# Kernel optimization log

Hardware: AMD Instinct MI355X
Metric: run time of the kernel (lower is better)

The kernel has to match this reference:

```python
import jax, jax.numpy as jnp
import numpy as np

HEAD_SIZE = 128
BLOCK_SIZE = 2048


def setup_inputs() -> dict:
    key = jax.random.key(0)
    kx, kk, kq, kv = jax.random.split(key, 4)
    B, T, C = 8, 2048, HEAD_SIZE
    s = 1.0 / np.sqrt(C)
    x = jax.random.normal(kx, (B, T, C), dtype=jnp.float32)
    Wk = jax.random.normal(kk, (C, C), dtype=jnp.float32) * s
    Wq = jax.random.normal(kq, (C, C), dtype=jnp.float32) * s
    Wv = jax.random.normal(kv, (C, C), dtype=jnp.float32) * s
    return {"x": x, "Wk": Wk, "Wq": Wq, "Wv": Wv}


def reference(x, Wk, Wq, Wv):
    B, T, C = x.shape
    # nn.Linear(C, C, bias=False): y = x @ W.T
    k = jnp.einsum('btc,dc->btd', x, Wk)
    q = jnp.einsum('btc,dc->btd', x, Wq)
    v = jnp.einsum('btc,dc->btd', x, Wv)
    scores = jnp.einsum('btd,bsd->bts', q, k) * (C ** -0.5)  # [B,T,T]
    causal = jnp.tril(jnp.ones((T, T), dtype=bool))
    scores = jnp.where(causal, scores, -jnp.inf)
    weights = jax.nn.softmax(scores, axis=-1)
    return jnp.einsum('bts,bsd->btd', weights, v)
```

## Files before the change

kernel.cpp:

```cpp
#include <hip/hip_runtime.h>

#define T_SEQ 2048
#define C_DIM 128
#define S_QK 0.08838834764831845f

typedef __attribute__((ext_vector_type(8))) short bf16x8;
typedef __attribute__((ext_vector_type(4))) float f32x4;

#define OPART_OFF 12582912UL
#define ML_OFF    31457280UL

#define GLOAD_LDS16(gp, lp)                                          \
    __builtin_amdgcn_global_load_lds(                                \
        (const __attribute__((address_space(1))) void*)(gp),         \
        (__attribute__((address_space(3))) void*)(lp), 16, 0, 0)

__device__ __forceinline__ unsigned short f2bf(float f) {
    union { float f; unsigned int u; } v; v.f = f;
    unsigned int r = v.u + 0x7FFFu + ((v.u >> 16) & 1u);
    return (unsigned short)(r >> 16);
}

__device__ __forceinline__ int chunk_base(int qt) {
    int g = qt >> 3;
    if (g == 1) return (qt - 8) * 2;
    if (g == 2) return 16 + (qt - 16) * 3;
    return 40 + (qt - 24) * 4;
}

__global__ __launch_bounds__(256) void proj_kernel(
    const float* __restrict__ x,
    const float* __restrict__ Wk, const float* __restrict__ Wq,
    const float* __restrict__ Wv,
    unsigned short* __restrict__ qo, unsigned short* __restrict__ ko,
    unsigned short* __restrict__ vto)
{
    const int rt = blockIdx.x;
    const int z  = blockIdx.y;
    const int tid  = threadIdx.x;
    const int lane = tid & 63;
    const int w    = tid >> 6;
    const int n16  = lane & 15;
    const int quad = lane >> 4;

    __shared__ __align__(16) unsigned short Wl[128 * 136];
    __shared__ __align__(16) unsigned short Xl[9216];

    const float* Wsrc = (z == 0 ? Wq : z == 1 ? Wk : Wv);
    const float wscale = (z == 0) ? S_QK : 1.0f;
    #pragma unroll
    for (int i = 0; i < 16; ++i) {
        int e = (tid + i * 256) * 4;
        int r = e >> 7, c = e & 127;
        float4 v = *reinterpret_cast<const float4*>(Wsrc + e);
        ushort4 o4;
        o4.x = f2bf(v.x * wscale); o4.y = f2bf(v.y * wscale);
        o4.z = f2bf(v.z * wscale); o4.w = f2bf(v.w * wscale);
        *reinterpret_cast<ushort4*>(&Wl[r * 136 + c]) = o4;
    }
    const float* xrow = x + (size_t)rt * 64 * C_DIM;
    #pragma unroll
    for (int i = 0; i < 8; ++i) {
        int e = (tid + i * 256) * 4;
        int r = e >> 7, c = e & 127;
        float4 v = *reinterpret_cast<const float4*>(xrow + e);
        ushort4 o4;
        o4.x = f2bf(v.x); o4.y = f2bf(v.y);
        o4.z = f2bf(v.z); o4.w = f2bf(v.w);
        *reinterpret_cast<ushort4*>(&Xl[r * 136 + c]) = o4;
    }
    __syncthreads();

    const int arow = w * 16 + n16;
    bf16x8 afr[4];
    #pragma unroll
    for (int kk = 0; kk < 4; ++kk)
        afr[kk] = *reinterpret_cast<const bf16x8*>(&Xl[arow * 136 + kk * 32 + quad * 8]);

    f32x4 acc[8];
    #pragma unroll
    for (int nt = 0; nt < 8; ++nt) acc[nt] = (f32x4){0.f, 0.f, 0.f, 0.f};
    #pragma unroll
    for (int kk = 0; kk < 4; ++kk)
        #pragma unroll
        for (int nt = 0; nt < 8; ++nt) {
            bf16x8 bfr = *reinterpret_cast<const bf16x8*>(
                &Wl[(nt * 16 + n16) * 136 + kk * 32 + quad * 8]);
            acc[nt] = __builtin_amdgcn_mfma_f32_16x16x32_bf16(afr[kk], bfr, acc[nt], 0, 0, 0);
        }

    const int trow_base = w * 16 + quad * 4;
    __syncthreads();
    if (z < 2) {
        #pragma unroll
        for (int nt = 0; nt < 8; ++nt)
            #pragma unroll
            for (int r = 0; r < 4; ++r)
                Xl[(trow_base + r) * 136 + nt * 16 + n16] = f2bf(acc[nt][r]);
        __syncthreads();
        unsigned short* dst = (z == 0 ? qo : ko) + (size_t)rt * 64 * C_DIM;
        #pragma unroll
        for (int i = 0; i < 4; ++i) {
            int e = (tid + i * 256) * 8;
            int r = e >> 7, c = e & 127;
            *reinterpret_cast<uint4*>(dst + e) =
                *reinterpret_cast<const uint4*>(&Xl[r * 136 + c]);
        }
    } else {
        const int b  = rt >> 5;
        const int qt = rt & 31;
        #pragma unroll
        for (int nt = 0; nt < 8; ++nt)
            #pragma unroll
            for (int r = 0; r < 4; ++r)
                Xl[(nt * 16 + n16) * 72 + trow_base + r] = f2bf(acc[nt][r]);
        __syncthreads();
        unsigned short* dst = vto + (size_t)b * C_DIM * T_SEQ + (size_t)qt * 64;
        #pragma unroll
        for (int i = 0; i < 4; ++i) {
            int e = tid + i * 256;
            int d = e >> 3, cv = (e & 7) * 8;
            *reinterpret_cast<uint4*>(dst + (size_t)d * T_SEQ + cv) =
                *reinterpret_cast<const uint4*>(&Xl[d * 72 + cv]);
        }
    }
}

__device__ __forceinline__ void stage_tile(
    const char* ksb, const char* vsb,
    unsigned short* klbuf, unsigned short* vlbuf, int tid, int w)
{
    #pragma unroll
    for (int it = 0; it < 4; ++it) {
        const int L = it * 256 + tid;
        const int r = L >> 4, c = L & 15;
        GLOAD_LDS16(ksb + r * 256 + ((c ^ (r & 7)) << 4),
                    klbuf + (size_t)(it * 256 + w * 64) * 8);
    }
    #pragma unroll
    for (int it = 0; it < 4; ++it) {
        const int L = it * 256 + tid;
        const int r = L >> 3, c = L & 7;
        GLOAD_LDS16(vsb + (size_t)r * (T_SEQ * 2) + ((c ^ (r & 7)) << 4),
                    vlbuf + (size_t)(it * 256 + w * 64) * 8);
    }
}

__global__ __launch_bounds__(256) void attn_kernel(
    const unsigned short* __restrict__ qb,
    const unsigned short* __restrict__ kb,
    const unsigned short* __restrict__ vtb,
    float* __restrict__ opart, float2* __restrict__ mlbuf,
    float* __restrict__ out)
{
    const int lin   = blockIdx.x;
    const int b     = lin & 7;
    const int rest  = lin >> 3;
    const int qt    = rest & 31;
    const int chunk = rest >> 5;
    if (chunk * 8 > qt) return;

    const int tid  = threadIdx.x;
    const int lane = tid & 63;
    const int w    = tid >> 6;
    const int n16  = lane & 15;
    const int quad = lane >> 4;

    __shared__ __align__(16) unsigned short Kl[2][64 * 128];
    __shared__ __align__(16) unsigned short Vl[2][128 * 64];
    __shared__ __align__(16) unsigned short Pl[4][16 * 72];

    const size_t bT = (size_t)b * T_SEQ;
    const int qbase = qt * 64 + w * 16;
    const int k0 = chunk * 8;
    const int k1 = min(k0 + 8, qt + 1);

    const char* kbase = (const char*)(kb + bT * C_DIM);
    const char* vbase = (const char*)(vtb + (size_t)b * C_DIM * T_SEQ);

    stage_tile(kbase + (size_t)k0 * 64 * 256, vbase + (size_t)k0 * 128,
               Kl[0], Vl[0], tid, w);

    bf16x8 qfr[4];
    #pragma unroll
    for (int kk = 0; kk < 4; ++kk)
        qfr[kk] = *reinterpret_cast<const bf16x8*>(
            qb + (bT + qbase + n16) * C_DIM + kk * 32 + quad * 8);

    f32x4 o[8];
    #pragma unroll
    for (int ct = 0; ct < 8; ++ct) o[ct] = (f32x4){0.f, 0.f, 0.f, 0.f};
    float m[4], l[4];
    #pragma unroll
    for (int r = 0; r < 4; ++r) { m[r] = -INFINITY; l[r] = 0.f; }

    int cur = 0;
    for (int kt = k0; kt < k1; ++kt, cur ^= 1) {
        if (kt + 1 < k1) {
            stage_tile(kbase + (size_t)(kt + 1) * 64 * 256,
                       vbase + (size_t)(kt + 1) * 128,
                       Kl[cur ^ 1], Vl[cur ^ 1], tid, w);
            asm volatile("s_waitcnt vmcnt(8)" ::: "memory");
        } else {
            asm volatile("s_waitcnt vmcnt(0)" ::: "memory");
        }
        __builtin_amdgcn_s_barrier();

        const unsigned short* klc = Kl[cur];
        const unsigned short* vlc = Vl[cur];

        f32x4 s[4];
        #pragma unroll
        for (int nt = 0; nt < 4; ++nt) s[nt] = (f32x4){0.f, 0.f, 0.f, 0.f};
        #pragma unroll
        for (int kk = 0; kk < 4; ++kk)
            #pragma unroll
            for (int nt = 0; nt < 4; ++nt) {
                const int rr = nt * 16 + n16;
                const int p  = (kk * 4 + quad) ^ (n16 & 7);
                bf16x8 bfr = *reinterpret_cast<const bf16x8*>(&klc[rr * 128 + p * 8]);
                s[nt] = __builtin_amdgcn_mfma_f32_16x16x32_bf16(qfr[kk], bfr, s[nt], 0, 0, 0);
            }

        if (kt == qt) {
            #pragma unroll
            for (int nt = 0; nt < 4; ++nt)
                #pragma unroll
                for (int r = 0; r < 4; ++r) {
                    int sabs = kt * 64 + nt * 16 + n16;
                    int qabs = qbase + quad * 4 + r;
                    if (sabs > qabs) s[nt][r] = -1e30f;
                }
        }

        float alpha[4];
        #pragma unroll
        for (int r = 0; r < 4; ++r) {
            float tmax = fmaxf(fmaxf(s[0][r], s[1][r]), fmaxf(s[2][r], s[3][r]));
            #pragma unroll
            for (int off = 1; off < 16; off <<= 1)
                tmax = fmaxf(tmax, __shfl_xor(tmax, off));
            float mn = fmaxf(m[r], tmax);
            alpha[r] = __expf(m[r] - mn);
            float tsum = 0.f;
            #pragma unroll
            for (int nt = 0; nt < 4; ++nt) {
                float p = __expf(s[nt][r] - mn);
                s[nt][r] = p;
                tsum += p;
            }
            #pragma unroll
            for (int off = 1; off < 16; off <<= 1)
                tsum += __shfl_xor(tsum, off);
            l[r] = l[r] * alpha[r] + tsum;
            m[r] = mn;
        }
        #pragma unroll
        for (int ct = 0; ct < 8; ++ct)
            #pragma unroll
            for (int r = 0; r < 4; ++r)
                o[ct][r] *= alpha[r];

        unsigned short* pw = Pl[w];
        #pragma unroll
        for (int nt = 0; nt < 4; ++nt)
            #pragma unroll
            for (int r = 0; r < 4; ++r)
                pw[(quad * 4 + r) * 72 + nt * 16 + n16] = f2bf(s[nt][r]);

        #pragma unroll
        for (int kk2 = 0; kk2 < 2; ++kk2) {
            bf16x8 afr = *reinterpret_cast<const bf16x8*>(
                &pw[n16 * 72 + kk2 * 32 + quad * 8]);
            #pragma unroll
            for (int ct = 0; ct < 8; ++ct) {
                const int rv = ct * 16 + n16;
                const int p  = (kk2 * 4 + quad) ^ (n16 & 7);
                bf16x8 bfr = *reinterpret_cast<const bf16x8*>(&vlc[rv * 64 + p * 8]);
                o[ct] = __builtin_amdgcn_mfma_f32_16x16x32_bf16(afr, bfr, o[ct], 0, 0, 0);
            }
        }

        asm volatile("s_waitcnt lgkmcnt(0)" ::: "memory");
        __builtin_amdgcn_s_barrier();
    }

    if (qt < 8) {
        float* outp = out + (bT + qbase) * C_DIM;
        #pragma unroll
        for (int r = 0; r < 4; ++r) {
            float inv = 1.0f / l[r];
            #pragma unroll
            for (int ct = 0; ct < 8; ++ct)
                outp[(size_t)(quad * 4 + r) * C_DIM + ct * 16 + n16] = o[ct][r] * inv;
        }
    } else {
        const int slot = b * 72 + chunk_base(qt) + chunk;
        float* op = opart + (size_t)slot * 8192;
        #pragma unroll
        for (int r = 0; r < 4; ++r) {
            int row = w * 16 + quad * 4 + r;
            #pragma unroll
            for (int ct = 0; ct < 8; ++ct)
                op[row * 128 + ct * 16 + n16] = o[ct][r];
            if (n16 == 0)
                mlbuf[(size_t)slot * 64 + row] = make_float2(m[r], l[r]);
        }
    }
}

__global__ __launch_bounds__(256) void merge_kernel(
    const float* __restrict__ opart, const float2* __restrict__ mlbuf,
    float* __restrict__ out)
{
    const int qt = 8 + blockIdx.x;
    const int b  = blockIdx.y;
    const int nch  = (qt >> 3) + 1;
    const int base = b * 72 + chunk_base(qt);
    const int row = threadIdx.x >> 2;
    const int c0  = (threadIdx.x & 3) * 32;

    float mi[4], li[4], wgt[4];
    float M = -INFINITY;
    for (int i = 0; i < nch; ++i) {
        float2 t = mlbuf[(size_t)(base + i) * 64 + row];
        mi[i] = t.x; li[i] = t.y;
        M = fmaxf(M, t.x);
    }
    float L = 0.f;
    for (int i = 0; i < nch; ++i) {
        wgt[i] = __expf(mi[i] - M);
        L += li[i] * wgt[i];
    }
    const float inv = 1.0f / L;

    float* orow = out + ((size_t)(b * T_SEQ + qt * 64 + row)) * C_DIM;
    #pragma unroll
    for (int j = 0; j < 8; ++j) {
        int col = c0 + j * 4;
        float ax = 0.f, ay = 0.f, az = 0.f, aw = 0.f;
        for (int i = 0; i < nch; ++i) {
            float4 p = *reinterpret_cast<const float4*>(
                opart + (size_t)(base + i) * 8192 + row * 128 + col);
            ax += wgt[i] * p.x; ay += wgt[i] * p.y;
            az += wgt[i] * p.z; aw += wgt[i] * p.w;
        }
        float4 r4; r4.x = ax * inv; r4.y = ay * inv; r4.z = az * inv; r4.w = aw * inv;
        *reinterpret_cast<float4*>(orow + col) = r4;
    }
}

extern "C" void kernel_launch(void* const* d_in, const int* in_sizes, int n_in,
                              void* d_out, int out_size, void* d_ws, size_t ws_size,
                              hipStream_t stream) {
    const float* x  = (const float*)d_in[0];
    const float* Wk = (const float*)d_in[1];
    const float* Wq = (const float*)d_in[2];
    const float* Wv = (const float*)d_in[3];

    unsigned short* qw  = (unsigned short*)d_ws;
    unsigned short* kw  = qw + 2097152;
    unsigned short* vw  = kw + 2097152;
    float*          opart = (float*)((char*)d_ws + OPART_OFF);
    float2*         mlb   = (float2*)((char*)d_ws + ML_OFF);

    proj_kernel<<<dim3(256, 3), 256, 0, stream>>>(x, Wk, Wq, Wv, qw, kw, vw);
    attn_kernel<<<dim3(1024), 256, 0, stream>>>(qw, kw, vw, opart, mlb, (float*)d_out);
    merge_kernel<<<dim3(24, 8), 256, 0, stream>>>(opart, mlb, (float*)d_out);
}
```

Baseline: 125.1 us.

## Transpose attention MFMA orientation and halve KV tile to raise occupancy

Swaps the MFMA operand order so each lane owns one query row, which lets the softmax row max and sum use two cross-quad shuffles instead of four-step reductions per row. The KV tile shrinks from 64 to 32 keys, which halves shared memory so that launch bounds can request four blocks per CU. The V tile gets a new XOR swizzle, and outputs and partials are written as float4. The trade-off is twice as many loop iterations and barriers per chunk, each doing less MFMA work.

```diff
diff --git a/kernel.cpp b/kernel.cpp
--- a/kernel.cpp
+++ b/kernel.cpp
@@ -126,27 +126,28 @@
     }
 }
 
-__device__ __forceinline__ void stage_tile(
+__device__ __forceinline__ void stage_tile32(
     const char* ksb, const char* vsb,
     unsigned short* klbuf, unsigned short* vlbuf, int tid, int w)
 {
     #pragma unroll
-    for (int it = 0; it < 4; ++it) {
+    for (int it = 0; it < 2; ++it) {
         const int L = it * 256 + tid;
         const int r = L >> 4, c = L & 15;
         GLOAD_LDS16(ksb + r * 256 + ((c ^ (r & 7)) << 4),
                     klbuf + (size_t)(it * 256 + w * 64) * 8);
     }
     #pragma unroll
-    for (int it = 0; it < 4; ++it) {
+    for (int it = 0; it < 2; ++it) {
         const int L = it * 256 + tid;
-        const int r = L >> 3, c = L & 7;
-        GLOAD_LDS16(vsb + (size_t)r * (T_SEQ * 2) + ((c ^ (r & 7)) << 4),
+        const int r = L >> 2, c = L & 3;
+        GLOAD_LDS16(vsb + (size_t)r * (T_SEQ * 2) +
+                        ((c ^ (r & 3) ^ ((r >> 2) & 3)) << 4),
                     vlbuf + (size_t)(it * 256 + w * 64) * 8);
     }
 }
 
-__global__ __launch_bounds__(256) void attn_kernel(
+__global__ __launch_bounds__(256, 4) void attn_kernel(
     const unsigned short* __restrict__ qb,
     const unsigned short* __restrict__ kb,
     const unsigned short* __restrict__ vtb,
@@ -166,20 +167,22 @@
     const int n16  = lane & 15;
     const int quad = lane >> 4;
 
-    __shared__ __align__(16) unsigned short Kl[2][64 * 128];
-    __shared__ __align__(16) unsigned short Vl[2][128 * 64];
-    __shared__ __align__(16) unsigned short Pl[4][16 * 72];
+    __shared__ __align__(16) unsigned short Kl[2][32 * 128];
+    __shared__ __align__(16) unsigned short Vl[2][128 * 32];
+    __shared__ __align__(16) unsigned short Pl[4][16 * 40];
 
     const size_t bT = (size_t)b * T_SEQ;
     const int qbase = qt * 64 + w * 16;
-    const int k0 = chunk * 8;
-    const int k1 = min(k0 + 8, qt + 1);
+    const int qabs  = qbase + n16;
+
+    const int st0 = chunk * 16;
+    const int st1 = min(chunk * 16 + 16, 2 * qt + 2);
 
     const char* kbase = (const char*)(kb + bT * C_DIM);
     const char* vbase = (const char*)(vtb + (size_t)b * C_DIM * T_SEQ);
 
-    stage_tile(kbase + (size_t)k0 * 64 * 256, vbase + (size_t)k0 * 128,
-               Kl[0], Vl[0], tid, w);
+    stage_tile32(kbase + (size_t)st0 * 8192, vbase + (size_t)st0 * 64,
+                 Kl[0], Vl[0], tid, w);
 
     bf16x8 qfr[4];
     #pragma unroll
@@ -190,17 +193,18 @@
     f32x4 o[8];
     #pragma unroll
     for (int ct = 0; ct < 8; ++ct) o[ct] = (f32x4){0.f, 0.f, 0.f, 0.f};
-    float m[4], l[4];
-    #pragma unroll
-    for (int r = 0; r < 4; ++r) { m[r] = -INFINITY; l[r] = 0.f; }
+    float m_ = -INFINITY, l_ = 0.f;
+
+    unsigned short* pw = Pl[w];
+    const int vswz = (quad ^ (n16 & 3) ^ ((n16 >> 2) & 3)) * 8;
 
     int cur = 0;
-    for (int kt = k0; kt < k1; ++kt, cur ^= 1) {
-        if (kt + 1 < k1) {
-            stage_tile(kbase + (size_t)(kt + 1) * 64 * 256,
-                       vbase + (size_t)(kt + 1) * 128,
-                       Kl[cur ^ 1], Vl[cur ^ 1], tid, w);
-            asm volatile("s_waitcnt vmcnt(8)" ::: "memory");
+    for (int st = st0; st < st1; ++st, cur ^= 1) {
+        if (st + 1 < st1) {
+            stage_tile32(kbase + (size_t)(st + 1) * 8192,
+                         vbase + (size_t)(st + 1) * 64,
+                         Kl[cur ^ 1], Vl[cur ^ 1], tid, w);
+            asm volatile("s_waitcnt vmcnt(4)" ::: "memory");
         } else {
             asm volatile("s_waitcnt vmcnt(0)" ::: "memory");
         }
@@ -209,76 +213,67 @@
         const unsigned short* klc = Kl[cur];
         const unsigned short* vlc = Vl[cur];
 
-        f32x4 s[4];
-        #pragma unroll
-        for (int nt = 0; nt < 4; ++nt) s[nt] = (f32x4){0.f, 0.f, 0.f, 0.f};
+        f32x4 s[2];
+        s[0] = (f32x4){0.f, 0.f, 0.f, 0.f};
+        s[1] = (f32x4){0.f, 0.f, 0.f, 0.f};
         #pragma unroll
         for (int kk = 0; kk < 4; ++kk)
             #pragma unroll
-            for (int nt = 0; nt < 4; ++nt) {
-                const int rr = nt * 16 + n16;
-                const int p  = (kk * 4 + quad) ^ (n16 & 7);
-                bf16x8 bfr = *reinterpret_cast<const bf16x8*>(&klc[rr * 128 + p * 8]);
-                s[nt] = __builtin_amdgcn_mfma_f32_16x16x32_bf16(qfr[kk], bfr, s[nt], 0, 0, 0);
+            for (int nt = 0; nt < 2; ++nt) {
+                bf16x8 kfr = *reinterpret_cast<const bf16x8*>(
+                    &klc[(nt * 16 + n16) * 128 + (((kk * 4 + quad) ^ (n16 & 7)) * 8)]);
+                s[nt] = __builtin_amdgcn_mfma_f32_16x16x32_bf16(kfr, qfr[kk], s[nt], 0, 0, 0);
             }
 
-        if (kt == qt) {
-            #pragma unroll
-            for (int nt = 0; nt < 4; ++nt)
+        if (st >= 2 * qt) {
+            #pragma unroll
+            for (int nt = 0; nt < 2; ++nt)
                 #pragma unroll
                 for (int r = 0; r < 4; ++r) {
-                    int sabs = kt * 64 + nt * 16 + n16;
-                    int qabs = qbase + quad * 4 + r;
+                    int sabs = st * 32 + nt * 16 + quad * 4 + r;
                     if (sabs > qabs) s[nt][r] = -1e30f;
                 }
         }
 
-        float alpha[4];
-        #pragma unroll
-        for (int r = 0; r < 4; ++r) {
-            float tmax = fmaxf(fmaxf(s[0][r], s[1][r]), fmaxf(s[2][r], s[3][r]));
-            #pragma unroll
-            for (int off = 1; off < 16; off <<= 1)
-                tmax = fmaxf(tmax, __shfl_xor(tmax, off));
-            float mn = fmaxf(m[r], tmax);
-            alpha[r] = __expf(m[r] - mn);
-            float tsum = 0.f;
-            #pragma unroll
-            for (int nt = 0; nt < 4; ++nt) {
+        float pmax = fmaxf(fmaxf(fmaxf(s[0][0], s[0][1]), fmaxf(s[0][2], s[0][3])),
+                           fmaxf(fmaxf(s[1][0], s[1][1]), fmaxf(s[1][2], s[1][3])));
+        pmax = fmaxf(pmax, __shfl_xor(pmax, 16));
+        pmax = fmaxf(pmax, __shfl_xor(pmax, 32));
+        float mn = fmaxf(m_, pmax);
+        float alpha = __expf(m_ - mn);
+        float tsum = 0.f;
+        #pragma unroll
+        for (int nt = 0; nt < 2; ++nt)
+            #pragma unroll
+            for (int r = 0; r < 4; ++r) {
                 float p = __expf(s[nt][r] - mn);
                 s[nt][r] = p;
                 tsum += p;
             }
-            #pragma unroll
-            for (int off = 1; off < 16; off <<= 1)
-                tsum += __shfl_xor(tsum, off);
-            l[r] = l[r] * alpha[r] + tsum;
-            m[r] = mn;
-        }
-        #pragma unroll
-        for (int ct = 0; ct < 8; ++ct)
-            #pragma unroll
-            for (int r = 0; r < 4; ++r)
-                o[ct][r] *= alpha[r];
-
-        unsigned short* pw = Pl[w];
-        #pragma unroll
-        for (int nt = 0; nt < 4; ++nt)
-            #pragma unroll
-            for (int r = 0; r < 4; ++r)
-                pw[(quad * 4 + r) * 72 + nt * 16 + n16] = f2bf(s[nt][r]);
-
-        #pragma unroll
-        for (int kk2 = 0; kk2 < 2; ++kk2) {
-            bf16x8 afr = *reinterpret_cast<const bf16x8*>(
-                &pw[n16 * 72 + kk2 * 32 + quad * 8]);
-            #pragma unroll
-            for (int ct = 0; ct < 8; ++ct) {
-                const int rv = ct * 16 + n16;
-                const int p  = (kk2 * 4 + quad) ^ (n16 & 7);
-                bf16x8 bfr = *reinterpret_cast<const bf16x8*>(&vlc[rv * 64 + p * 8]);
-                o[ct] = __builtin_amdgcn_mfma_f32_16x16x32_bf16(afr, bfr, o[ct], 0, 0, 0);
-            }
+        tsum += __shfl_xor(tsum, 16);
+        tsum += __shfl_xor(tsum, 32);
+        l_ = l_ * alpha + tsum;
+        m_ = mn;
+        #pragma unroll
+        for (int ct = 0; ct < 8; ++ct) {
+            o[ct][0] *= alpha; o[ct][1] *= alpha;
+            o[ct][2] *= alpha; o[ct][3] *= alpha;
+        }
+
+        #pragma unroll
+        for (int nt = 0; nt < 2; ++nt) {
+            ushort4 pk;
+            pk.x = f2bf(s[nt][0]); pk.y = f2bf(s[nt][1]);
+            pk.z = f2bf(s[nt][2]); pk.w = f2bf(s[nt][3]);
+            *reinterpret_cast<ushort4*>(&pw[n16 * 40 + nt * 16 + quad * 4]) = pk;
+        }
+
+        bf16x8 pfr = *reinterpret_cast<const bf16x8*>(&pw[n16 * 40 + quad * 8]);
+        #pragma unroll
+        for (int ct = 0; ct < 8; ++ct) {
+            bf16x8 vfr = *reinterpret_cast<const bf16x8*>(
+                &vlc[(ct * 16 + n16) * 32 + vswz]);
+            o[ct] = __builtin_amdgcn_mfma_f32_16x16x32_bf16(vfr, pfr, o[ct], 0, 0, 0);
         }
 
         asm volatile("s_waitcnt lgkmcnt(0)" ::: "memory");
@@ -286,26 +281,27 @@
     }
 
     if (qt < 8) {
-        float* outp = out + (bT + qbase) * C_DIM;
-        #pragma unroll
-        for (int r = 0; r < 4; ++r) {
-            float inv = 1.0f / l[r];
-            #pragma unroll
-            for (int ct = 0; ct < 8; ++ct)
-                outp[(size_t)(quad * 4 + r) * C_DIM + ct * 16 + n16] = o[ct][r] * inv;
+        float* outp = out + (bT + qbase + n16) * C_DIM;
+        const float inv = 1.0f / l_;
+        #pragma unroll
+        for (int ct = 0; ct < 8; ++ct) {
+            float4 r4;
+            r4.x = o[ct][0] * inv; r4.y = o[ct][1] * inv;
+            r4.z = o[ct][2] * inv; r4.w = o[ct][3] * inv;
+            *reinterpret_cast<float4*>(outp + ct * 16 + quad * 4) = r4;
         }
     } else {
         const int slot = b * 72 + chunk_base(qt) + chunk;
-        float* op = opart + (size_t)slot * 8192;
-        #pragma unroll
-        for (int r = 0; r < 4; ++r) {
-            int row = w * 16 + quad * 4 + r;
-            #pragma unroll
-            for (int ct = 0; ct < 8; ++ct)
-                op[row * 128 + ct * 16 + n16] = o[ct][r];
-            if (n16 == 0)
-                mlbuf[(size_t)slot * 64 + row] = make_float2(m[r], l[r]);
-        }
+        float* op = opart + (size_t)slot * 8192 + (size_t)(w * 16 + n16) * 128;
+        #pragma unroll
+        for (int ct = 0; ct < 8; ++ct) {
+            float4 r4;
+            r4.x = o[ct][0]; r4.y = o[ct][1];
+            r4.z = o[ct][2]; r4.w = o[ct][3];
+            *reinterpret_cast<float4*>(op + ct * 16 + quad * 4) = r4;
+        }
+        if (quad == 0)
+            mlbuf[(size_t)slot * 64 + w * 16 + n16] = make_float2(m_, l_);
     }
 }
 
```

After: 122.6 us. No clear change (-2.0%).
